# Optimization experiments

Measured on AMD Instinct MI355X. Metric: run time of the kernel, lower is better.

Reference implementation:

```python
import jax, jax.numpy as jnp
import numpy as np

B, S, D_IN, D_OUT = 4, 2048, 2048, 8192


def setup_inputs() -> dict:
    key = jax.random.key(0)
    k1, k2 = jax.random.split(key)
    x = jax.random.normal(k1, (B, S, D_IN), dtype=jnp.float32)
    weight = jax.random.normal(k2, (D_OUT, D_IN), dtype=jnp.float32) * 0.02
    alpha = jnp.float32(1.0)
    bias = jnp.zeros((D_OUT,), dtype=jnp.float32)
    return {"x": x, "weight": weight, "alpha": alpha, "bias": bias}


def reference(x, weight, alpha, bias):
    # Ternary quantization: delta = 0.7 * mean(|w|); w_q in {-1,0,1} * alpha
    delta = 0.7 * jnp.mean(jnp.abs(weight))
    w_t = jnp.where(weight > delta, jnp.float32(1.0),
                    jnp.where(weight < -delta, jnp.float32(-1.0), jnp.float32(0.0)))
    w_q = w_t * alpha  # [out, in]
    # F.linear: x @ w_q^T + bias
    return jnp.einsum('bsd,od->bso', x, w_q) + bias
```

## Files before the change

### kernel.cpp

```cpp
#include <hip/hip_runtime.h>
#include <hip/hip_bf16.h>
#include <stdint.h>

typedef __attribute__((ext_vector_type(4))) int i32x4;
typedef __attribute__((ext_vector_type(16))) int i32x16;
typedef signed char s8;

#define M_TOT 8192
#define N_TOT 8192
#define K_TOT 2048
#define W_COUNT (N_TOT * K_TOT)
#define X_COUNT (M_TOT * K_TOT)

__global__ void tl_reduce(const float* __restrict__ w, const float* __restrict__ x,
                          double* __restrict__ wsum, float* __restrict__ xmax) {
    const int b = blockIdx.x;
    if (b < 1024) {
        const int tid = b * 256 + threadIdx.x;
        const float4* w4 = (const float4*)w;
        double s = 0.0;
        for (int i = tid; i < W_COUNT / 4; i += 1024 * 256) {
            float4 v = w4[i];
            s += (double)fabsf(v.x) + (double)fabsf(v.y) + (double)fabsf(v.z) + (double)fabsf(v.w);
        }
        #pragma unroll
        for (int off = 32; off > 0; off >>= 1) s += __shfl_down(s, off);
        __shared__ double red[4];
        if ((threadIdx.x & 63) == 0) red[threadIdx.x >> 6] = s;
        __syncthreads();
        if (threadIdx.x == 0) wsum[b] = (red[0] + red[1]) + (red[2] + red[3]);
    } else {
        const int tid = (b - 1024) * 256 + threadIdx.x;
        const float4* x4 = (const float4*)x;
        float m = 0.0f;
        for (int i = tid; i < X_COUNT / 4; i += 1024 * 256) {
            float4 v = x4[i];
            m = fmaxf(m, fmaxf(fmaxf(fabsf(v.x), fabsf(v.y)), fmaxf(fabsf(v.z), fabsf(v.w))));
        }
        #pragma unroll
        for (int off = 32; off > 0; off >>= 1) m = fmaxf(m, __shfl_down(m, off));
        __shared__ float redm[4];
        if ((threadIdx.x & 63) == 0) redm[threadIdx.x >> 6] = m;
        __syncthreads();
        if (threadIdx.x == 0) xmax[b - 1024] = fmaxf(fmaxf(redm[0], redm[1]), fmaxf(redm[2], redm[3]));
    }
}

__global__ void tl_finalize(const double* __restrict__ wsum, const float* __restrict__ xmax,
                            const float* __restrict__ alpha,
                            double* __restrict__ delta, float* __restrict__ qp) {
    const int t = threadIdx.x;
    double s = (wsum[t] + wsum[t + 256]) + (wsum[t + 512] + wsum[t + 768]);
    float m = fmaxf(fmaxf(xmax[t], xmax[t + 256]), fmaxf(xmax[t + 512], xmax[t + 768]));
    #pragma unroll
    for (int off = 32; off > 0; off >>= 1) {
        s += __shfl_down(s, off);
        m = fmaxf(m, __shfl_down(m, off));
    }
    __shared__ double rs[4];
    __shared__ float rm[4];
    if ((t & 63) == 0) { rs[t >> 6] = s; rm[t >> 6] = m; }
    __syncthreads();
    if (t == 0) {
        *delta = 0.7 * (((rs[0] + rs[1]) + (rs[2] + rs[3])) / (double)W_COUNT);
        float mm = fmaxf(fmaxf(rm[0], rm[1]), fmaxf(rm[2], rm[3]));
        qp[0] = 127.0f / mm;
        qp[1] = alpha[0] * (mm / 127.0f);
    }
}

__global__ void tl_tern_w(const float* __restrict__ w, const double* __restrict__ delta_p,
                          s8* __restrict__ wb) {
    const double d = *delta_p;
    const int i = (blockIdx.x * 256 + threadIdx.x) * 16;
    union { s8 c[16]; i32x4 v; } o;
    #pragma unroll
    for (int j = 0; j < 16; j += 4) {
        float4 v = *(const float4*)(w + i + j);
        float f[4] = {v.x, v.y, v.z, v.w};
        #pragma unroll
        for (int r = 0; r < 4; ++r) {
            double wd = (double)f[r];
            o.c[j + r] = wd > d ? 1 : (wd < -d ? -1 : 0);
        }
    }
    *(i32x4*)(wb + i) = o.v;
}

__global__ void tl_quant_x(const float* __restrict__ x, const float* __restrict__ qp,
                           s8* __restrict__ xb) {
    const float inv = qp[0];
    const int i = (blockIdx.x * 256 + threadIdx.x) * 16;
    union { s8 c[16]; i32x4 v; } o;
    #pragma unroll
    for (int j = 0; j < 16; j += 4) {
        float4 v = *(const float4*)(x + i + j);
        float f[4] = {v.x, v.y, v.z, v.w};
        #pragma unroll
        for (int r = 0; r < 4; ++r) {
            int q = (int)__builtin_rintf(f[r] * inv);
            q = q > 127 ? 127 : (q < -127 ? -127 : q);
            o.c[j + r] = (s8)q;
        }
    }
    *(i32x4*)(xb + i) = o.v;
}


#define SB    __builtin_amdgcn_sched_barrier(0)
#define BARR  __builtin_amdgcn_s_barrier()
#define LGKM6 asm volatile("s_waitcnt lgkmcnt(6)" ::: "memory")
#define LGKM0 asm volatile("s_waitcnt lgkmcnt(0)" ::: "memory")
#define VMW(N) asm volatile("s_waitcnt vmcnt(" #N ")" ::: "memory")

#define GLDS(SRC, DOFF) __builtin_amdgcn_global_load_lds(                      \
    (const __attribute__((address_space(1))) void*)(SRC),                      \
    (__attribute__((address_space(3))) void*)(lds + (DOFF)), 16, 0, 0)

#define RD6(AR, BR, S, KK) do {                                                \
    _Pragma("unroll") for (int m_ = 0; m_ < 4; ++m_)                           \
        AR[m_] = *(const i32x4*)(lds + (S) * 16384 + wrOff + m_ * 2048 +       \
                                 (lrd ^ ((KK) * 32)));                         \
    _Pragma("unroll") for (int n_ = 0; n_ < 2; ++n_)                           \
        BR[n_] = *(const i32x4*)(lds + 49152 + (S) * 16384 + wcOff + n_ * 2048 + \
                                 (lrd ^ ((KK) * 32)));                         \
} while (0)

#define MM(AR, BR) do {                                                        \
    _Pragma("unroll") for (int m_ = 0; m_ < 4; ++m_)                           \
    _Pragma("unroll") for (int n_ = 0; n_ < 2; ++n_)                           \
        acc[m_][n_] = __builtin_amdgcn_mfma_i32_32x32x32_i8(                   \
            AR[m_], BR[n_], acc[m_][n_], 0, 0, 0);                             \
} while (0)

#define STG_A(SS, KOFF) do {                                                   \
    GLDS(aSrc + (KOFF), (SS) * 16384 + L);                                     \
    GLDS(aSrc + (KOFF) + 262144, (SS) * 16384 + 8192 + L);                     \
} while (0)
#define STG_B(SS, KOFF) do {                                                   \
    GLDS(bSrc + (KOFF), 49152 + (SS) * 16384 + L);                             \
    GLDS(bSrc + (KOFF) + 262144, 49152 + (SS) * 16384 + 8192 + L);             \
} while (0)

#define KTILE(S, SN, SG, KOFF, DOSTG, GATE, DONEXT) do {                       \
    RD6(aO, bO, S, 1);                                                         \
    LGKM6; SB;                                                                 \
    MM(aE, bE);                                                                \
    if (DOSTG) { STG_A(SG, KOFF); STG_B(SG, KOFF); }                           \
    LGKM0; SB;                                                                 \
    GATE; SB;                                                                  \
    BARR;                                                                      \
    if (DONEXT) RD6(aE, bE, SN, 0);                                            \
    MM(aO, bO);                                                                \
} while (0)

__global__ __launch_bounds__(512, 2) void tl_gemm_i8(
    const s8* __restrict__ A, const s8* __restrict__ Bm,
    const float* __restrict__ qp, const float* __restrict__ bias,
    float* __restrict__ C) {
    __shared__ __attribute__((aligned(128))) char lds[98304];

    const int t = threadIdx.x;
    const int wid = t >> 6;
    const int l = t & 63;
    const int wr = wid >> 2;
    const int wc = wid & 3;

    const int bid = blockIdx.x;
    const int xc = bid & 7;
    const int j = bid >> 3;
    const int tm = xc * 4 + ((j >> 3) & 3);
    const int tn = (j >> 5) * 8 + (j & 7);
    const int row0 = tm * 256, col0 = tn * 256;

    const int L = t * 16;
    const int off = L ^ (((L >> 7) & 3) << 4);
    const int sr = off >> 6;
    const int kb = off & 63;
    const s8* aSrc = A + (size_t)(row0 + sr) * K_TOT + kb;
    const s8* bSrc = Bm + (size_t)(col0 + sr) * K_TOT + kb;

    const int rl = l & 31, kg = l >> 5;
    const int lrd = rl * 64 + ((kg ^ ((rl >> 1) & 3)) << 4);
    const int wrOff = wr * 8192;
    const int wcOff = wc * 4096;

    i32x16 acc[4][2] = {};
    i32x4 aE[4], bE[2], aO[4], bO[2];

    STG_A(0, 0); STG_B(0, 0);
    STG_A(1, 64); STG_B(1, 64);
    VMW(4); SB; BARR;
    RD6(aE, bE, 0, 0);

    int koff = 128;
    #pragma unroll 1
    for (int i = 0; i < 10; ++i) {
        KTILE(0, 1, 2, koff, 1, VMW(4), 1); koff += 64;
        KTILE(1, 2, 0, koff, 1, VMW(4), 1); koff += 64;
        KTILE(2, 0, 1, koff, 1, VMW(4), 1); koff += 64;
    }
    KTILE(0, 1, 0, 0, 0, VMW(0), 1);
    KTILE(1, 0, 0, 0, 0, (void)0, 0);

    const float osc = qp[1];
    #pragma unroll
    for (int m_ = 0; m_ < 4; ++m_) {
        const int crow = row0 + wr * 128 + m_ * 32 + kg * 4;
        #pragma unroll
        for (int n_ = 0; n_ < 2; ++n_) {
            const int ccol = col0 + wc * 64 + n_ * 32 + rl;
            const float bv = bias[ccol];
            #pragma unroll
            for (int r = 0; r < 16; ++r) {
                const int row = crow + (r & 3) + 8 * (r >> 2);
                C[(size_t)row * N_TOT + ccol] = (float)acc[m_][n_][r] * osc + bv;
            }
        }
    }
}

extern "C" void kernel_launch(void* const* d_in, const int* in_sizes, int n_in,
                              void* d_out, int out_size, void* d_ws, size_t ws_size,
                              hipStream_t stream) {
    const float* x     = (const float*)d_in[0];
    const float* wgt   = (const float*)d_in[1];
    const float* alpha = (const float*)d_in[2];
    const float* bias  = (const float*)d_in[3];
    float* out = (float*)d_out;

    char* ws = (char*)d_ws;
    double* wsum = (double*)ws;
    float* xmax  = (float*)(ws + 8192);
    double* delta = (double*)(ws + 12288);
    float* qp     = (float*)(ws + 12304);
    s8* xb = (s8*)(ws + 16384);
    s8* wb = (s8*)(ws + 16384 + (size_t)X_COUNT);

    tl_reduce<<<2048, 256, 0, stream>>>(wgt, x, wsum, xmax);
    tl_finalize<<<1, 256, 0, stream>>>(wsum, xmax, alpha, delta, qp);
    tl_tern_w<<<W_COUNT / (256 * 16), 256, 0, stream>>>(wgt, delta, wb);
    tl_quant_x<<<X_COUNT / (256 * 16), 256, 0, stream>>>(x, qp, xb);
    tl_gemm_i8<<<(M_TOT / 256) * (N_TOT / 256), 512, 0, stream>>>(xb, wb, qp, bias, out);
}
```

Before: 202.8 us.

## Use 128-wide K tiles with double-buffered LDS and fuse quantization kernels

```diff
diff --git a/kernel.cpp b/kernel.cpp
--- a/kernel.cpp
+++ b/kernel.cpp
@@ -69,41 +69,42 @@
     }
 }
 
-__global__ void tl_tern_w(const float* __restrict__ w, const double* __restrict__ delta_p,
-                          s8* __restrict__ wb) {
-    const double d = *delta_p;
-    const int i = (blockIdx.x * 256 + threadIdx.x) * 16;
-    union { s8 c[16]; i32x4 v; } o;
-    #pragma unroll
-    for (int j = 0; j < 16; j += 4) {
-        float4 v = *(const float4*)(w + i + j);
-        float f[4] = {v.x, v.y, v.z, v.w};
-        #pragma unroll
-        for (int r = 0; r < 4; ++r) {
-            double wd = (double)f[r];
-            o.c[j + r] = wd > d ? 1 : (wd < -d ? -1 : 0);
-        }
-    }
-    *(i32x4*)(wb + i) = o.v;
-}
-
-__global__ void tl_quant_x(const float* __restrict__ x, const float* __restrict__ qp,
-                           s8* __restrict__ xb) {
-    const float inv = qp[0];
-    const int i = (blockIdx.x * 256 + threadIdx.x) * 16;
-    union { s8 c[16]; i32x4 v; } o;
-    #pragma unroll
-    for (int j = 0; j < 16; j += 4) {
-        float4 v = *(const float4*)(x + i + j);
-        float f[4] = {v.x, v.y, v.z, v.w};
-        #pragma unroll
-        for (int r = 0; r < 4; ++r) {
-            int q = (int)__builtin_rintf(f[r] * inv);
-            q = q > 127 ? 127 : (q < -127 ? -127 : q);
-            o.c[j + r] = (s8)q;
-        }
-    }
-    *(i32x4*)(xb + i) = o.v;
+__global__ void tl_quant(const float* __restrict__ w, const float* __restrict__ x,
+                         const double* __restrict__ delta_p, const float* __restrict__ qp,
+                         s8* __restrict__ wb, s8* __restrict__ xb) {
+    const int b = blockIdx.x;
+    if (b < 4096) {
+        const double d = *delta_p;
+        const int i = (b * 256 + threadIdx.x) * 16;
+        union { s8 c[16]; i32x4 v; } o;
+        #pragma unroll
+        for (int j = 0; j < 16; j += 4) {
+            float4 v = *(const float4*)(w + i + j);
+            float f[4] = {v.x, v.y, v.z, v.w};
+            #pragma unroll
+            for (int r = 0; r < 4; ++r) {
+                double wd = (double)f[r];
+                o.c[j + r] = wd > d ? 1 : (wd < -d ? -1 : 0);
+            }
+        }
+        *(i32x4*)(wb + i) = o.v;
+    } else {
+        const float inv = qp[0];
+        const int i = ((b - 4096) * 256 + threadIdx.x) * 16;
+        union { s8 c[16]; i32x4 v; } o;
+        #pragma unroll
+        for (int j = 0; j < 16; j += 4) {
+            float4 v = *(const float4*)(x + i + j);
+            float f[4] = {v.x, v.y, v.z, v.w};
+            #pragma unroll
+            for (int r = 0; r < 4; ++r) {
+                int q = (int)__builtin_rintf(f[r] * inv);
+                q = q > 127 ? 127 : (q < -127 ? -127 : q);
+                o.c[j + r] = (s8)q;
+            }
+        }
+        *(i32x4*)(xb + i) = o.v;
+    }
 }
 
 
@@ -117,48 +118,57 @@
     (const __attribute__((address_space(1))) void*)(SRC),                      \
     (__attribute__((address_space(3))) void*)(lds + (DOFF)), 16, 0, 0)
 
-#define RD6(AR, BR, S, KK) do {                                                \
+#define RD6(AR, BR, SA, SB_, Q) do {                                           \
     _Pragma("unroll") for (int m_ = 0; m_ < 4; ++m_)                           \
-        AR[m_] = *(const i32x4*)(lds + (S) * 16384 + wrOff + m_ * 2048 +       \
-                                 (lrd ^ ((KK) * 32)));                         \
+        AR[m_] = *(const i32x4*)(lds + (SA) + wrOff + m_ * 4096 +              \
+                                 (((Q) * 32 + kg16) ^ xr));                    \
     _Pragma("unroll") for (int n_ = 0; n_ < 2; ++n_)                           \
-        BR[n_] = *(const i32x4*)(lds + 49152 + (S) * 16384 + wcOff + n_ * 2048 + \
-                                 (lrd ^ ((KK) * 32)));                         \
-} while (0)
-
-#define MM(AR, BR) do {                                                        \
+        BR[n_] = *(const i32x4*)(lds + (SB_) + wcOff + n_ * 4096 +             \
+                                 (((Q) * 32 + kg16) ^ xr));                    \
+} while (0)
+
+#define MM8(AR, BR) do {                                                       \
     _Pragma("unroll") for (int m_ = 0; m_ < 4; ++m_)                           \
     _Pragma("unroll") for (int n_ = 0; n_ < 2; ++n_)                           \
         acc[m_][n_] = __builtin_amdgcn_mfma_i32_32x32x32_i8(                   \
             AR[m_], BR[n_], acc[m_][n_], 0, 0, 0);                             \
 } while (0)
 
-#define STG_A(SS, KOFF) do {                                                   \
-    GLDS(aSrc + (KOFF), (SS) * 16384 + L);                                     \
-    GLDS(aSrc + (KOFF) + 262144, (SS) * 16384 + 8192 + L);                     \
-} while (0)
-#define STG_B(SS, KOFF) do {                                                   \
-    GLDS(bSrc + (KOFF), 49152 + (SS) * 16384 + L);                             \
-    GLDS(bSrc + (KOFF) + 262144, 49152 + (SS) * 16384 + 8192 + L);             \
-} while (0)
-
-#define KTILE(S, SN, SG, KOFF, DOSTG, GATE, DONEXT) do {                       \
-    RD6(aO, bO, S, 1);                                                         \
+#define STG_A2(DS, KOFF, J0) do {                                              \
+    GLDS(aSrc + (size_t)((J0) * 64) * K_TOT + (KOFF), (DS) + (J0) * 8192 + L); \
+    GLDS(aSrc + (size_t)(((J0) + 1) * 64) * K_TOT + (KOFF),                    \
+         (DS) + ((J0) + 1) * 8192 + L);                                        \
+} while (0)
+#define STG_B2(DS, KOFF, J0) do {                                              \
+    GLDS(bSrc + (size_t)((J0) * 64) * K_TOT + (KOFF), (DS) + (J0) * 8192 + L); \
+    GLDS(bSrc + (size_t)(((J0) + 1) * 64) * K_TOT + (KOFF),                    \
+         (DS) + ((J0) + 1) * 8192 + L);                                        \
+} while (0)
+
+#define KT(SA, SBs, SAN, SBN, KOFF, DOSTG, GATE, DONEXT) do {                  \
+    RD6(aO, bO, SA, SBs, 1);                                                   \
     LGKM6; SB;                                                                 \
-    MM(aE, bE);                                                                \
-    if (DOSTG) { STG_A(SG, KOFF); STG_B(SG, KOFF); }                           \
+    MM8(aE, bE);                                                       \
+    if (DOSTG) { STG_A2(SAN, KOFF, 0); STG_A2(SAN, KOFF, 2); }                 \
+    RD6(aE, bE, SA, SBs, 2);                                                   \
+    LGKM6; SB;                                                                 \
+    MM8(aO, bO);                                                       \
+    if (DOSTG) { STG_B2(SBN, KOFF, 0); STG_B2(SBN, KOFF, 2); }                 \
+    RD6(aO, bO, SA, SBs, 3);                                                   \
+    LGKM6; SB;                                                                 \
+    MM8(aE, bE);                                                       \
     LGKM0; SB;                                                                 \
     GATE; SB;                                                                  \
     BARR;                                                                      \
-    if (DONEXT) RD6(aE, bE, SN, 0);                                            \
-    MM(aO, bO);                                                                \
+    if (DONEXT) RD6(aE, bE, SAN, SBN, 0);                                      \
+    MM8(aO, bO);                                                       \
 } while (0)
 
 __global__ __launch_bounds__(512, 2) void tl_gemm_i8(
     const s8* __restrict__ A, const s8* __restrict__ Bm,
     const float* __restrict__ qp, const float* __restrict__ bias,
     float* __restrict__ C) {
-    __shared__ __attribute__((aligned(128))) char lds[98304];
+    __shared__ __attribute__((aligned(128))) char lds[131072];
 
     const int t = threadIdx.x;
     const int wid = t >> 6;
@@ -174,34 +184,33 @@
     const int row0 = tm * 256, col0 = tn * 256;
 
     const int L = t * 16;
-    const int off = L ^ (((L >> 7) & 3) << 4);
-    const int sr = off >> 6;
-    const int kb = off & 63;
+    const int sr = t >> 3;
+    const int kb = ((t & 7) << 4) ^ (((t >> 3) & 7) << 4);
     const s8* aSrc = A + (size_t)(row0 + sr) * K_TOT + kb;
     const s8* bSrc = Bm + (size_t)(col0 + sr) * K_TOT + kb;
 
     const int rl = l & 31, kg = l >> 5;
-    const int lrd = rl * 64 + ((kg ^ ((rl >> 1) & 3)) << 4);
-    const int wrOff = wr * 8192;
-    const int wcOff = wc * 4096;
+    const int kg16 = kg * 16;
+    const int xr = (rl & 7) << 4;
+    const int wrOff = wr * 128 * 128 + rl * 128;
+    const int wcOff = wc * 64 * 128 + rl * 128;
 
     i32x16 acc[4][2] = {};
     i32x4 aE[4], bE[2], aO[4], bO[2];
 
-    STG_A(0, 0); STG_B(0, 0);
-    STG_A(1, 64); STG_B(1, 64);
-    VMW(4); SB; BARR;
-    RD6(aE, bE, 0, 0);
+    STG_A2(0, 0, 0); STG_A2(0, 0, 2);
+    STG_B2(65536, 0, 0); STG_B2(65536, 0, 2);
+    VMW(0); SB; BARR;
+    RD6(aE, bE, 0, 65536, 0);
 
     int koff = 128;
     #pragma unroll 1
-    for (int i = 0; i < 10; ++i) {
-        KTILE(0, 1, 2, koff, 1, VMW(4), 1); koff += 64;
-        KTILE(1, 2, 0, koff, 1, VMW(4), 1); koff += 64;
-        KTILE(2, 0, 1, koff, 1, VMW(4), 1); koff += 64;
-    }
-    KTILE(0, 1, 0, 0, 0, VMW(0), 1);
-    KTILE(1, 0, 0, 0, 0, (void)0, 0);
+    for (int i = 0; i < 7; ++i) {
+        KT(0, 65536, 32768, 98304, koff, 1, VMW(0), 1); koff += 128;
+        KT(32768, 98304, 0, 65536, koff, 1, VMW(0), 1); koff += 128;
+    }
+    KT(0, 65536, 32768, 98304, koff, 1, VMW(0), 1);
+    KT(32768, 98304, 0, 65536, 0, 0, (void)0, 0);
 
     const float osc = qp[1];
     #pragma unroll
@@ -239,7 +248,6 @@
 
     tl_reduce<<<2048, 256, 0, stream>>>(wgt, x, wsum, xmax);
     tl_finalize<<<1, 256, 0, stream>>>(wsum, xmax, alpha, delta, qp);
-    tl_tern_w<<<W_COUNT / (256 * 16), 256, 0, stream>>>(wgt, delta, wb);
-    tl_quant_x<<<X_COUNT / (256 * 16), 256, 0, stream>>>(x, qp, xb);
+    tl_quant<<<8192, 256, 0, stream>>>(wgt, x, delta, qp, wb, xb);
     tl_gemm_i8<<<(M_TOT / 256) * (N_TOT / 256), 512, 0, stream>>>(xb, wb, qp, bias, out);
 }
```

After: 200.7 us. Within noise of the previous version (-1.1%).

## Interleave LDS fragment reads with MFMAs and merge quantization kernels

Applied to the files above, without the earlier changes.

```diff
diff --git a/kernel.cpp b/kernel.cpp
--- a/kernel.cpp
+++ b/kernel.cpp
@@ -69,68 +69,69 @@
     }
 }
 
-__global__ void tl_tern_w(const float* __restrict__ w, const double* __restrict__ delta_p,
-                          s8* __restrict__ wb) {
-    const double d = *delta_p;
-    const int i = (blockIdx.x * 256 + threadIdx.x) * 16;
-    union { s8 c[16]; i32x4 v; } o;
-    #pragma unroll
-    for (int j = 0; j < 16; j += 4) {
-        float4 v = *(const float4*)(w + i + j);
-        float f[4] = {v.x, v.y, v.z, v.w};
-        #pragma unroll
-        for (int r = 0; r < 4; ++r) {
-            double wd = (double)f[r];
-            o.c[j + r] = wd > d ? 1 : (wd < -d ? -1 : 0);
-        }
-    }
-    *(i32x4*)(wb + i) = o.v;
-}
-
-__global__ void tl_quant_x(const float* __restrict__ x, const float* __restrict__ qp,
-                           s8* __restrict__ xb) {
-    const float inv = qp[0];
-    const int i = (blockIdx.x * 256 + threadIdx.x) * 16;
-    union { s8 c[16]; i32x4 v; } o;
-    #pragma unroll
-    for (int j = 0; j < 16; j += 4) {
-        float4 v = *(const float4*)(x + i + j);
-        float f[4] = {v.x, v.y, v.z, v.w};
-        #pragma unroll
-        for (int r = 0; r < 4; ++r) {
-            int q = (int)__builtin_rintf(f[r] * inv);
-            q = q > 127 ? 127 : (q < -127 ? -127 : q);
-            o.c[j + r] = (s8)q;
-        }
-    }
-    *(i32x4*)(xb + i) = o.v;
+__global__ void tl_quant(const float* __restrict__ w, const float* __restrict__ x,
+                         const double* __restrict__ delta_p, const float* __restrict__ qp,
+                         s8* __restrict__ wb, s8* __restrict__ xb) {
+    const int b = blockIdx.x;
+    if (b < 4096) {
+        const double d = *delta_p;
+        const int i = (b * 256 + threadIdx.x) * 16;
+        union { s8 c[16]; i32x4 v; } o;
+        #pragma unroll
+        for (int j = 0; j < 16; j += 4) {
+            float4 v = *(const float4*)(w + i + j);
+            float f[4] = {v.x, v.y, v.z, v.w};
+            #pragma unroll
+            for (int r = 0; r < 4; ++r) {
+                double wd = (double)f[r];
+                o.c[j + r] = wd > d ? 1 : (wd < -d ? -1 : 0);
+            }
+        }
+        *(i32x4*)(wb + i) = o.v;
+    } else {
+        const float inv = qp[0];
+        const int i = ((b - 4096) * 256 + threadIdx.x) * 16;
+        union { s8 c[16]; i32x4 v; } o;
+        #pragma unroll
+        for (int j = 0; j < 16; j += 4) {
+            float4 v = *(const float4*)(x + i + j);
+            float f[4] = {v.x, v.y, v.z, v.w};
+            #pragma unroll
+            for (int r = 0; r < 4; ++r) {
+                int q = (int)__builtin_rintf(f[r] * inv);
+                q = q > 127 ? 127 : (q < -127 ? -127 : q);
+                o.c[j + r] = (s8)q;
+            }
+        }
+        *(i32x4*)(xb + i) = o.v;
+    }
 }
 
 
 #define SB    __builtin_amdgcn_sched_barrier(0)
 #define BARR  __builtin_amdgcn_s_barrier()
-#define LGKM6 asm volatile("s_waitcnt lgkmcnt(6)" ::: "memory")
-#define LGKM0 asm volatile("s_waitcnt lgkmcnt(0)" ::: "memory")
+#define LG(N) asm volatile("s_waitcnt lgkmcnt(" #N ")" ::: "memory")
 #define VMW(N) asm volatile("s_waitcnt vmcnt(" #N ")" ::: "memory")
 
 #define GLDS(SRC, DOFF) __builtin_amdgcn_global_load_lds(                      \
     (const __attribute__((address_space(1))) void*)(SRC),                      \
     (__attribute__((address_space(3))) void*)(lds + (DOFF)), 16, 0, 0)
 
-#define RD6(AR, BR, S, KK) do {                                                \
-    _Pragma("unroll") for (int m_ = 0; m_ < 4; ++m_)                           \
-        AR[m_] = *(const i32x4*)(lds + (S) * 16384 + wrOff + m_ * 2048 +       \
-                                 (lrd ^ ((KK) * 32)));                         \
-    _Pragma("unroll") for (int n_ = 0; n_ < 2; ++n_)                           \
-        BR[n_] = *(const i32x4*)(lds + 49152 + (S) * 16384 + wcOff + n_ * 2048 + \
-                                 (lrd ^ ((KK) * 32)));                         \
-} while (0)
-
-#define MM(AR, BR) do {                                                        \
-    _Pragma("unroll") for (int m_ = 0; m_ < 4; ++m_)                           \
-    _Pragma("unroll") for (int n_ = 0; n_ < 2; ++n_)                           \
-        acc[m_][n_] = __builtin_amdgcn_mfma_i32_32x32x32_i8(                   \
-            AR[m_], BR[n_], acc[m_][n_], 0, 0, 0);                             \
+#define RD_B(BR_, S, KK) do {                                                  \
+    BR_[0] = *(const i32x4*)(lds + 49152 + (S) * 16384 + wcOff + 0 * 2048 +    \
+                             (lrd ^ ((KK) * 32)));                             \
+    BR_[1] = *(const i32x4*)(lds + 49152 + (S) * 16384 + wcOff + 1 * 2048 +    \
+                             (lrd ^ ((KK) * 32)));                             \
+} while (0)
+#define RD_A1(AR_, I_, S, KK)                                                  \
+    AR_[I_] = *(const i32x4*)(lds + (S) * 16384 + wrOff + (I_) * 2048 +        \
+                              (lrd ^ ((KK) * 32)))
+
+#define MM2(AR_, BR_, M_) do {                                                 \
+    acc[M_][0] = __builtin_amdgcn_mfma_i32_32x32x32_i8(                        \
+        AR_[M_], BR_[0], acc[M_][0], 0, 0, 0);                                 \
+    acc[M_][1] = __builtin_amdgcn_mfma_i32_32x32x32_i8(                        \
+        AR_[M_], BR_[1], acc[M_][1], 0, 0, 0);                                 \
 } while (0)
 
 #define STG_A(SS, KOFF) do {                                                   \
@@ -142,16 +143,43 @@
     GLDS(bSrc + (KOFF) + 262144, 49152 + (SS) * 16384 + 8192 + L);             \
 } while (0)
 
-#define KTILE(S, SN, SG, KOFF, DOSTG, GATE, DONEXT) do {                       \
-    RD6(aO, bO, S, 1);                                                         \
-    LGKM6; SB;                                                                 \
-    MM(aE, bE);                                                                \
+#define KTILE_F(S, SN, SG, KOFF, DOSTG, GATE) do {                             \
+    LG(3); SB;                                        \
+    MM2(aE, bE, 0);                                                            \
+    RD_B(bO, S, 1); SB;                                           \
+    LG(4); SB;                                                        \
+    MM2(aE, bE, 1);                                                            \
+    RD_A1(aO, 0, S, 1); RD_A1(aO, 1, S, 1); SB;                   \
+    LG(5); SB;                                                        \
+    MM2(aE, bE, 2);                                                            \
+    RD_A1(aO, 2, S, 1); RD_A1(aO, 3, S, 1); SB;                   \
     if (DOSTG) { STG_A(SG, KOFF); STG_B(SG, KOFF); }                           \
-    LGKM0; SB;                                                                 \
+    SB;                                                                        \
+    LG(6); SB;                                                        \
+    MM2(aE, bE, 3);                                                            \
     GATE; SB;                                                                  \
     BARR;                                                                      \
-    if (DONEXT) RD6(aE, bE, SN, 0);                                            \
-    MM(aO, bO);                                                                \
+    RD_B(bE, SN, 0);                                                           \
+    RD_A1(aE, 0, SN, 0); RD_A1(aE, 1, SN, 0);                                  \
+    RD_A1(aE, 2, SN, 0); RD_A1(aE, 3, SN, 0); SB;                \
+    LG(9); SB; MM2(aO, bO, 0);                                \
+    LG(8); SB; MM2(aO, bO, 1);                                                 \
+    LG(7); SB; MM2(aO, bO, 2);                                                 \
+    LG(6); SB; MM2(aO, bO, 3);                          \
+} while (0)
+
+#define KTILE_LAST(S) do {                                                     \
+    LG(3); SB; MM2(aE, bE, 0);                                                 \
+    RD_B(bO, S, 1); SB;                                                        \
+    LG(4); SB; MM2(aE, bE, 1);                                                 \
+    RD_A1(aO, 0, S, 1); RD_A1(aO, 1, S, 1); SB;                                \
+    LG(5); SB; MM2(aE, bE, 2);                                                 \
+    RD_A1(aO, 2, S, 1); RD_A1(aO, 3, S, 1); SB;                                \
+    LG(6); SB; MM2(aE, bE, 3);                                                 \
+    LG(3); SB; MM2(aO, bO, 0);                                                 \
+    LG(2); SB; MM2(aO, bO, 1);                                                 \
+    LG(1); SB; MM2(aO, bO, 2);                                                 \
+    LG(0); SB; MM2(aO, bO, 3);                                                 \
 } while (0)
 
 __global__ __launch_bounds__(512, 2) void tl_gemm_i8(
@@ -191,17 +219,19 @@
     STG_A(0, 0); STG_B(0, 0);
     STG_A(1, 64); STG_B(1, 64);
     VMW(4); SB; BARR;
-    RD6(aE, bE, 0, 0);
+    RD_B(bE, 0, 0);
+    RD_A1(aE, 0, 0, 0); RD_A1(aE, 1, 0, 0);
+    RD_A1(aE, 2, 0, 0); RD_A1(aE, 3, 0, 0); SB;
 
     int koff = 128;
     #pragma unroll 1
     for (int i = 0; i < 10; ++i) {
-        KTILE(0, 1, 2, koff, 1, VMW(4), 1); koff += 64;
-        KTILE(1, 2, 0, koff, 1, VMW(4), 1); koff += 64;
-        KTILE(2, 0, 1, koff, 1, VMW(4), 1); koff += 64;
-    }
-    KTILE(0, 1, 0, 0, 0, VMW(0), 1);
-    KTILE(1, 0, 0, 0, 0, (void)0, 0);
+        KTILE_F(0, 1, 2, koff, 1, VMW(4)); koff += 64;
+        KTILE_F(1, 2, 0, koff, 1, VMW(4)); koff += 64;
+        KTILE_F(2, 0, 1, koff, 1, VMW(4)); koff += 64;
+    }
+    KTILE_F(0, 1, 0, 0, 0, VMW(0));
+    KTILE_LAST(1);
 
     const float osc = qp[1];
     #pragma unroll
@@ -239,7 +269,6 @@
 
     tl_reduce<<<2048, 256, 0, stream>>>(wgt, x, wsum, xmax);
     tl_finalize<<<1, 256, 0, stream>>>(wsum, xmax, alpha, delta, qp);
-    tl_tern_w<<<W_COUNT / (256 * 16), 256, 0, stream>>>(wgt, delta, wb);
-    tl_quant_x<<<X_COUNT / (256 * 16), 256, 0, stream>>>(x, qp, xb);
+    tl_quant<<<8192, 256, 0, stream>>>(wgt, x, delta, qp, wb, xb);
     tl_gemm_i8<<<(M_TOT / 256) * (N_TOT / 256), 512, 0, stream>>>(xb, wb, qp, bias, out);
 }
```

Result: no change. 204.4 us (+0.8%).
